# Performance work log

Hardware: AMD Instinct MI355X
Metric: run time of the kernel (lower is better)

The kernel has to match this reference:

```python
import jax, jax.numpy as jnp
import numpy as np

EMBED = 64
HEADS = 8
HEAD_DIM = EMBED // HEADS
B, N, T = 8, 128, 64


def setup_inputs() -> dict:
    key = jax.random.key(0)
    ks = jax.random.split(key, 8)
    shp = (B, N, T, EMBED)
    values = jax.random.normal(ks[0], shp, dtype=jnp.float32)
    keys = jax.random.normal(ks[1], shp, dtype=jnp.float32)
    query = jax.random.normal(ks[2], shp, dtype=jnp.float32)
    s = 1.0 / np.sqrt(HEAD_DIM)
    Wv = jax.random.normal(ks[3], (HEAD_DIM, HEAD_DIM), dtype=jnp.float32) * s
    Wk = jax.random.normal(ks[4], (HEAD_DIM, HEAD_DIM), dtype=jnp.float32) * s
    Wq = jax.random.normal(ks[5], (HEAD_DIM, HEAD_DIM), dtype=jnp.float32) * s
    so = 1.0 / np.sqrt(EMBED)
    Wo = jax.random.normal(ks[6], (EMBED, EMBED), dtype=jnp.float32) * so
    bo = jax.random.normal(ks[7], (EMBED,), dtype=jnp.float32) * 0.01
    return {"values": values, "keys": keys, "query": query,
            "Wv": Wv, "Wk": Wk, "Wq": Wq, "Wo": Wo, "bo": bo}


def reference(values, keys, query, Wv, Wk, Wq, Wo, bo):
    b, n, t, c = query.shape
    h, d = HEADS, HEAD_DIM
    # split heads: (B,N,T,H,D)
    v = values.reshape(b, n, t, h, d)
    k = keys.reshape(b, n, t, h, d)
    q = query.reshape(b, n, t, h, d)
    # per-head linear projections (torch Linear: x @ W.T, no bias)
    v = jnp.einsum('bnthd,ed->bnthe', v, Wv)
    k = jnp.einsum('bnthd,ed->bnthe', k, Wk)
    q = jnp.einsum('bnthd,ed->bnthe', q, Wq)
    # attention over spatial axis N, independent per (t, h)
    energy = jnp.einsum('bqthd,bkthd->bqkth', q, k)  # (B,N,N,T,H)
    attn = jax.nn.softmax(energy / jnp.sqrt(jnp.float32(c)), axis=2)
    out = jnp.einsum('bqkth,bkthd->bqthd', attn, v).reshape(b, n, t, h * d)
    # fc_out: x @ Wo.T + bo
    return out @ Wo.T + bo
```

## Files before the change

kernel.cpp:

```cpp
#include <hip/hip_runtime.h>


typedef _Float16 half4 __attribute__((ext_vector_type(4)));
typedef __fp16   fp16x2 __attribute__((ext_vector_type(2)));
typedef float    f32x4 __attribute__((ext_vector_type(4)));

#define MFMA16(a,b,c) __builtin_amdgcn_mfma_f32_16x16x16f16((a),(b),(c),0,0,0)

__device__ __forceinline__ unsigned short f2h(float f){
    union { _Float16 h; unsigned short u; } c; c.h = (_Float16)f; return c.u;
}
__device__ __forceinline__ unsigned int pk2(float a, float b){
    union { fp16x2 h; unsigned int u; } c;
    c.h = __builtin_amdgcn_cvt_pkrtz(a, b);
    return c.u;
}

#define ZS 0
#define KB 8
#define QB 8200
#define VB 16392
#define CB 24584
#define WB 33800
#define LDS_TOTAL 38408

__global__ __launch_bounds__(512, 4)
void sattn_kernel(const float* __restrict__ V,
                  const float* __restrict__ K,
                  const float* __restrict__ Q,
                  const float* __restrict__ Wv,
                  const float* __restrict__ Wk,
                  const float* __restrict__ Wq,
                  const float* __restrict__ Wo,
                  const float* __restrict__ bo,
                  float* __restrict__ Out)
{
    __shared__ __align__(16) unsigned short smem[LDS_TOTAL];

    const int tid  = threadIdx.x;
    const int bid  = blockIdx.x;
    const int b    = bid >> 6;
    const int t    = bid & 63;
    const long base = (long)b * 524288 + t * 64;
    const float SC = 0.18033688011112043f;

    if (tid < 4) *(unsigned int*)(smem + tid*2) = 0u;

    {
        int o = tid >> 3, c8 = tid & 7;
        const float* ws = Wo + o*64 + c8*8;
        float4 a = *(const float4*)ws;
        float4 d = *(const float4*)(ws + 4);
        *(uint4*)(smem + WB + o*72 + c8*8) =
            make_uint4(pk2(a.x,a.y), pk2(a.z,a.w), pk2(d.x,d.y), pk2(d.z,d.w));
    }

    {
        float4 L[12];
        int cn_[2], ch_[2];
        #pragma unroll
        for (int i = 0; i < 2; ++i){
            int id = i*512 + tid;
            int cn = id >> 3, ch = id & 7;
            cn_[i] = cn; ch_[i] = ch;
            const float* pk = K + base + cn*4096 + ch*8;
            const float* pv = V + base + cn*4096 + ch*8;
            const float* pq = Q + base + cn*4096 + ch*8;
            L[i*6+0] = *(const float4*)pk;  L[i*6+1] = *(const float4*)(pk+4);
            L[i*6+2] = *(const float4*)pv;  L[i*6+3] = *(const float4*)(pv+4);
            L[i*6+4] = *(const float4*)pq;  L[i*6+5] = *(const float4*)(pq+4);
        }
        #pragma unroll
        for (int i = 0; i < 2; ++i){
            int cn = cn_[i], ch = ch_[i];
            float4 ka = L[i*6+0], kb = L[i*6+1];
            float4 va = L[i*6+2], vb = L[i*6+3];
            float4 qa = L[i*6+4], qb = L[i*6+5];
            float ok[8], ov[8], oq[8];
            #pragma unroll
            for (int e = 0; e < 8; ++e){
                float4 wk0 = *(const float4*)(Wk + e*8), wk1 = *(const float4*)(Wk + e*8 + 4);
                float4 wv0 = *(const float4*)(Wv + e*8), wv1 = *(const float4*)(Wv + e*8 + 4);
                float4 wq0 = *(const float4*)(Wq + e*8), wq1 = *(const float4*)(Wq + e*8 + 4);
                ok[e] = ka.x*wk0.x + ka.y*wk0.y + ka.z*wk0.z + ka.w*wk0.w
                      + kb.x*wk1.x + kb.y*wk1.y + kb.z*wk1.z + kb.w*wk1.w;
                ov[e] = va.x*wv0.x + va.y*wv0.y + va.z*wv0.z + va.w*wv0.w
                      + vb.x*wv1.x + vb.y*wv1.y + vb.z*wv1.z + vb.w*wv1.w;
                oq[e] = (qa.x*wq0.x + qa.y*wq0.y + qa.z*wq0.z + qa.w*wq0.w
                      +  qb.x*wq1.x + qb.y*wq1.y + qb.z*wq1.z + qb.w*wq1.w) * SC;
            }
            *(uint4*)(smem + KB + ch*1024 + cn*8) =
                make_uint4(pk2(ok[0],ok[1]), pk2(ok[2],ok[3]), pk2(ok[4],ok[5]), pk2(ok[6],ok[7]));
            *(uint4*)(smem + QB + ch*1024 + cn*8) =
                make_uint4(pk2(oq[0],oq[1]), pk2(oq[2],oq[3]), pk2(oq[4],oq[5]), pk2(oq[6],oq[7]));
            #pragma unroll
            for (int e = 0; e < 8; ++e)
                smem[VB + ch*1024 + e*128 + cn] = f2h(ov[e]);
        }
    }

    __syncthreads();

    const int h    = tid >> 6;
    const int q16  = tid & 15;
    const int quad = (tid & 63) >> 4;
    const f32x4 zz = {0.f, 0.f, 0.f, 0.f};

    half4 kf[8];
    #pragma unroll
    for (int mt = 0; mt < 8; ++mt){
        int a = KB + h*1024 + (mt*16 + q16)*8 + quad*4;
        if (quad >= 2) a = ZS;
        kf[mt] = *(const half4*)(smem + a);
    }
    half4 vf[8];
    #pragma unroll
    for (int s = 0; s < 8; ++s){
        int a = VB + h*1024 + q16*128 + s*16 + quad*4;
        if (q16 >= 8) a = ZS;
        vf[s] = *(const half4*)(smem + a);
    }
    half4 qf[8];
    #pragma unroll
    for (int qs = 0; qs < 8; ++qs){
        int a = QB + h*1024 + (qs*16 + q16)*8 + quad*4;
        if (quad >= 2) a = ZS;
        qf[qs] = *(const half4*)(smem + a);
    }

    #pragma unroll 1
    for (int qs = 0; qs < 8; ++qs){
        f32x4 acc[8];
        #pragma unroll
        for (int mt = 0; mt < 8; ++mt)
            acc[mt] = MFMA16(kf[mt], qf[qs], zz);

        float s = 0.f;
        #pragma unroll
        for (int mt = 0; mt < 8; ++mt){
            #pragma unroll
            for (int r = 0; r < 4; ++r){
                float p = __builtin_amdgcn_exp2f(fminf(acc[mt][r], 14.f));
                acc[mt][r] = p;
                s += p;
            }
        }

        union { uint2 u; half4 hp; } pf[8];
        #pragma unroll
        for (int mt = 0; mt < 8; ++mt)
            pf[mt].u = make_uint2(pk2(acc[mt][0], acc[mt][1]),
                                  pk2(acc[mt][2], acc[mt][3]));

        s += __shfl_xor(s, 16, 64);
        s += __shfl_xor(s, 32, 64);
        float inv = 1.0f / s;
        float invr[4];
        #pragma unroll
        for (int r = 0; r < 4; ++r)
            invr[r] = __shfl(inv, quad*4 + r, 64);

        f32x4 o = zz;
        #pragma unroll
        for (int s8 = 0; s8 < 8; ++s8)
            o = MFMA16(pf[s8].hp, vf[s8], o);

        if (q16 < 8){
            #pragma unroll
            for (int r = 0; r < 4; ++r){
                int row = qs*16 + quad*4 + r;
                smem[CB + row*72 + h*8 + q16] = f2h(o[r] * invr[r]);
            }
        }
    }

    __syncthreads();

    const int w = h;
    half4 af[4];
    #pragma unroll
    for (int ks = 0; ks < 4; ++ks)
        af[ks] = *(const half4*)(smem + CB + (w*16 + q16)*72 + ks*16 + quad*4);

    #pragma unroll
    for (int nt = 0; nt < 4; ++nt){
        f32x4 a = zz;
        #pragma unroll
        for (int ks = 0; ks < 4; ++ks){
            half4 bf = *(const half4*)(smem + WB + (nt*16 + q16)*72 + ks*16 + quad*4);
            a = MFMA16(af[ks], bf, a);
        }
        float bb = bo[nt*16 + q16];
        #pragma unroll
        for (int r = 0; r < 4; ++r){
            int row = w*16 + quad*4 + r;
            Out[base + (long)row*4096 + nt*16 + q16] = a[r] + bb;
        }
    }
}

extern "C" void kernel_launch(void* const* d_in, const int* in_sizes, int n_in,
                              void* d_out, int out_size, void* d_ws, size_t ws_size,
                              hipStream_t stream)
{
    const float* V  = (const float*)d_in[0];
    const float* K  = (const float*)d_in[1];
    const float* Q  = (const float*)d_in[2];
    const float* Wv = (const float*)d_in[3];
    const float* Wk = (const float*)d_in[4];
    const float* Wq = (const float*)d_in[5];
    const float* Wo = (const float*)d_in[6];
    const float* bo = (const float*)d_in[7];

    sattn_kernel<<<dim3(512), dim3(512), 0, stream>>>(
        V, K, Q, Wv, Wk, Wq, Wo, bo, (float*)d_out);
}
```

Measured before the change: 129.3 us.

## Defer softmax normalization to output projection and vectorize V staging stores

V is now stored to LDS with packed 16-byte writes in row layout, and each lane gathers its V fragment with scalar half loads. Softmax 1/sum factors are written to a small LDS table and applied to the attention output fragments just before the fc_out MFMA, which removes the per-row shuffles in the main loop. The logits get a constant -4 bias through the MFMA accumulator with a lower exp2 clamp, for fp16 range safety, and the PV accumulation is split into two independent chains to shorten the dependency. The risks are extra scalar LDS reads for V and fp16 rounding of unnormalized outputs and of the scale factors.

New measurement: 133.2 us. 3.0% more time.

```diff
diff --git a/kernel.cpp b/kernel.cpp
--- a/kernel.cpp
+++ b/kernel.cpp
@@ -22,7 +22,8 @@
 #define VB 16392
 #define CB 24584
 #define WB 33800
-#define LDS_TOTAL 38408
+#define IB 38408
+#define LDS_TOTAL 40456
 
 __global__ __launch_bounds__(512, 4)
 void sattn_kernel(const float* __restrict__ V,
@@ -36,6 +37,7 @@
                   float* __restrict__ Out)
 {
     __shared__ __align__(16) unsigned short smem[LDS_TOTAL];
+    const _Float16* sh = (const _Float16*)smem;
 
     const int tid  = threadIdx.x;
     const int bid  = blockIdx.x;
@@ -93,9 +95,8 @@
                 make_uint4(pk2(ok[0],ok[1]), pk2(ok[2],ok[3]), pk2(ok[4],ok[5]), pk2(ok[6],ok[7]));
             *(uint4*)(smem + QB + ch*1024 + cn*8) =
                 make_uint4(pk2(oq[0],oq[1]), pk2(oq[2],oq[3]), pk2(oq[4],oq[5]), pk2(oq[6],oq[7]));
-            #pragma unroll
-            for (int e = 0; e < 8; ++e)
-                smem[VB + ch*1024 + e*128 + cn] = f2h(ov[e]);
+            *(uint4*)(smem + VB + ch*1024 + cn*8) =
+                make_uint4(pk2(ov[0],ov[1]), pk2(ov[2],ov[3]), pk2(ov[4],ov[5]), pk2(ov[6],ov[7]));
         }
     }
 
@@ -105,6 +106,7 @@
     const int q16  = tid & 15;
     const int quad = (tid & 63) >> 4;
     const f32x4 zz = {0.f, 0.f, 0.f, 0.f};
+    const f32x4 m4 = {-4.f, -4.f, -4.f, -4.f};
 
     half4 kf[8];
     #pragma unroll
@@ -116,9 +118,14 @@
     half4 vf[8];
     #pragma unroll
     for (int s = 0; s < 8; ++s){
-        int a = VB + h*1024 + q16*128 + s*16 + quad*4;
-        if (q16 >= 8) a = ZS;
-        vf[s] = *(const half4*)(smem + a);
+        half4 vv;
+        #pragma unroll
+        for (int i = 0; i < 4; ++i){
+            int a = VB + h*1024 + (s*16 + quad*4 + i)*8 + q16;
+            if (q16 >= 8) a = ZS;
+            vv[i] = sh[a];
+        }
+        vf[s] = vv;
     }
     half4 qf[8];
     #pragma unroll
@@ -128,19 +135,21 @@
         qf[qs] = *(const half4*)(smem + a);
     }
 
+    float* invT = (float*)(smem + IB);
+
     #pragma unroll 1
     for (int qs = 0; qs < 8; ++qs){
         f32x4 acc[8];
         #pragma unroll
         for (int mt = 0; mt < 8; ++mt)
-            acc[mt] = MFMA16(kf[mt], qf[qs], zz);
+            acc[mt] = MFMA16(kf[mt], qf[qs], m4);
 
         float s = 0.f;
         #pragma unroll
         for (int mt = 0; mt < 8; ++mt){
             #pragma unroll
             for (int r = 0; r < 4; ++r){
-                float p = __builtin_amdgcn_exp2f(fminf(acc[mt][r], 14.f));
+                float p = __builtin_amdgcn_exp2f(fminf(acc[mt][r], 10.f));
                 acc[mt][r] = p;
                 s += p;
             }
@@ -155,21 +164,22 @@
         s += __shfl_xor(s, 16, 64);
         s += __shfl_xor(s, 32, 64);
         float inv = 1.0f / s;
-        float invr[4];
-        #pragma unroll
-        for (int r = 0; r < 4; ++r)
-            invr[r] = __shfl(inv, quad*4 + r, 64);
-
-        f32x4 o = zz;
-        #pragma unroll
-        for (int s8 = 0; s8 < 8; ++s8)
-            o = MFMA16(pf[s8].hp, vf[s8], o);
+        if (quad == 0)
+            invT[h*128 + qs*16 + q16] = inv;
+
+        f32x4 oa = zz, ob = zz;
+        #pragma unroll
+        for (int s8 = 0; s8 < 4; ++s8)
+            oa = MFMA16(pf[s8].hp, vf[s8], oa);
+        #pragma unroll
+        for (int s8 = 4; s8 < 8; ++s8)
+            ob = MFMA16(pf[s8].hp, vf[s8], ob);
 
         if (q16 < 8){
             #pragma unroll
             for (int r = 0; r < 4; ++r){
                 int row = qs*16 + quad*4 + r;
-                smem[CB + row*72 + h*8 + q16] = f2h(o[r] * invr[r]);
+                smem[CB + row*72 + h*8 + q16] = f2h(oa[r] + ob[r]);
             }
         }
     }
@@ -183,8 +193,16 @@
         af[ks] = *(const half4*)(smem + CB + (w*16 + q16)*72 + ks*16 + quad*4);
 
     #pragma unroll
+    for (int ks = 0; ks < 4; ++ks){
+        float svf = invT[(2*ks + (quad>>1))*128 + w*16 + q16];
+        _Float16 sv = (_Float16)svf;
+        half4 s4 = {sv, sv, sv, sv};
+        af[ks] *= s4;
+    }
+
+    #pragma unroll
     for (int nt = 0; nt < 4; ++nt){
-        f32x4 a = zz;
+        f32x4 a = {0.f, 0.f, 0.f, 0.f};
         #pragma unroll
         for (int ks = 0; ks < 4; ++ks){
             half4 bf = *(const half4*)(smem + WB + (nt*16 + q16)*72 + ks*16 + quad*4);
```
